# Kernel tuning notes

Measured on AMD Instinct MI355X. Metric: run time of the kernel, lower is better.

## Reference

```python
import jax, jax.numpy as jnp
import numpy as np

B, N, D = 64, 2048, 256
EPS = 1e-05


def setup_inputs() -> dict:
    key = jax.random.key(0)
    k1, k2 = jax.random.split(key)
    x = jax.random.normal(k1, (B, N, D), dtype=jnp.float32)
    lengths = jax.random.randint(k2, (B,), 1, N + 1, dtype=jnp.int32)
    weights = jnp.ones((D,), dtype=jnp.float32)
    biases = jnp.zeros((D,), dtype=jnp.float32)
    return {"x": x, "lengths": lengths, "weights": weights, "biases": biases}


def reference(x, lengths, weights, biases):
    # mask: [B, N, 1], 1.0 for valid set elements (idx < length)
    mask = (jnp.arange(N)[None, :] < lengths[:, None])[..., None].astype(x.dtype)
    denom = (lengths.astype(x.dtype) * D)  # [B]
    xm = x * mask
    means = jnp.sum(xm, axis=(1, 2)) / denom                      # [B]
    x_centered = (xm - means[:, None, None]) * mask               # [B,N,D]
    variances = jnp.sum(x_centered * x_centered, axis=(1, 2)) / denom  # [B]
    x_norm = x_centered / (jnp.sqrt(variances)[:, None, None] + EPS)
    # F.linear(x, diag_embed(w), b) == x * w + b (elementwise per-feature affine)
    out = (x_norm * weights + biases) * mask
    return out
```

## Files before the change

### kernel.cpp

```cpp
#include <hip/hip_runtime.h>


#define BB 64
#define NN 2048
#define DD 256
#define EPSV 1e-5f
#define CHUNKS 32
#define ROWS_PER_CHUNK (NN / CHUNKS)

typedef float f32x4 __attribute__((ext_vector_type(4)));

__global__ __launch_bounds__(256) void setnorm_partials(
    const float* __restrict__ x, const int* __restrict__ lengths,
    float* __restrict__ partials) {
  const int c = blockIdx.x;
  const int b = blockIdx.y;
  const int len = lengths[b];
  const int rowBase = c * ROWS_PER_CHUNK;
  int validRows = len - rowBase;
  if (validRows > ROWS_PER_CHUNK) validRows = ROWS_PER_CHUNK;

  float sum = 0.f, sumsq = 0.f;
  if (validRows > 0) {
    const f32x4* p =
        (const f32x4*)(x + ((size_t)b * NN + (size_t)rowBase) * DD);
    const int n4 = validRows * (DD / 4);
    for (int i = threadIdx.x; i < n4; i += 512) {
      f32x4 v = p[i];
      sum += v.x + v.y + v.z + v.w;
      sumsq += v.x * v.x + v.y * v.y + v.z * v.z + v.w * v.w;
      const int j = i + 256;
      if (j < n4) {
        f32x4 u = p[j];
        sum += u.x + u.y + u.z + u.w;
        sumsq += u.x * u.x + u.y * u.y + u.z * u.z + u.w * u.w;
      }
    }
  }
  #pragma unroll
  for (int off = 32; off > 0; off >>= 1) {
    sum += __shfl_down(sum, off, 64);
    sumsq += __shfl_down(sumsq, off, 64);
  }
  __shared__ float ssum[4], ssq[4];
  const int wave = threadIdx.x >> 6;
  const int lane = threadIdx.x & 63;
  if (lane == 0) { ssum[wave] = sum; ssq[wave] = sumsq; }
  __syncthreads();
  if (threadIdx.x == 0) {
    float ts = 0.f, tq = 0.f;
    #pragma unroll
    for (int w = 0; w < 4; ++w) { ts += ssum[w]; tq += ssq[w]; }
    partials[(b * CHUNKS + c) * 2 + 0] = ts;
    partials[(b * CHUNKS + c) * 2 + 1] = tq;
  }
}

__global__ __launch_bounds__(256) void setnorm_norm(
    const float* __restrict__ x, const int* __restrict__ lengths,
    const float* __restrict__ weights, const float* __restrict__ biases,
    const float* __restrict__ partials, float* __restrict__ out) {
  const int blockBase = blockIdx.x * 1024;
  const int b = blockBase >> 17;
  const int row0 = (blockBase & 131071) >> 6;
  const int len = lengths[b];

  if (row0 >= len) {
    const f32x4 z = {0.f, 0.f, 0.f, 0.f};
    #pragma unroll
    for (int i = 0; i < 4; ++i)
      __builtin_nontemporal_store(z,
          ((f32x4*)out) + blockBase + i * 256 + threadIdx.x);
    return;
  }

  __shared__ float s_mean, s_inv;
  if (threadIdx.x < 64) {
    float s = 0.f, q = 0.f;
    if (threadIdx.x < CHUNKS) {
      s = partials[(b * CHUNKS + threadIdx.x) * 2 + 0];
      q = partials[(b * CHUNKS + threadIdx.x) * 2 + 1];
    }
    #pragma unroll
    for (int off = 16; off > 0; off >>= 1) {
      s += __shfl_down(s, off, 64);
      q += __shfl_down(q, off, 64);
    }
    if (threadIdx.x == 0) {
      const float denom = (float)lengths[b] * (float)DD;
      const float mean = s / denom;
      float var = q / denom - mean * mean;
      var = fmaxf(var, 0.f);
      s_mean = mean;
      s_inv = 1.f / (sqrtf(var) + EPSV);
    }
  }
  __syncthreads();
  const float mean = s_mean;
  const float inv = s_inv;

  const int d4 = threadIdx.x & 63;
  const f32x4 w = ((const f32x4*)weights)[d4];
  const f32x4 bi = ((const f32x4*)biases)[d4];
  const int rowT = row0 + (threadIdx.x >> 6);

  #pragma unroll
  for (int i = 0; i < 4; ++i) {
    const int idx4 = blockBase + i * 256 + threadIdx.x;
    const int row = rowT + i * 4;
    f32x4 o = {0.f, 0.f, 0.f, 0.f};
    if (row < len) {
      const f32x4 v = ((const f32x4*)x)[idx4];
      o.x = (v.x - mean) * inv * w.x + bi.x;
      o.y = (v.y - mean) * inv * w.y + bi.y;
      o.z = (v.z - mean) * inv * w.z + bi.z;
      o.w = (v.w - mean) * inv * w.w + bi.w;
    }
    __builtin_nontemporal_store(o, ((f32x4*)out) + idx4);
  }
}

extern "C" void kernel_launch(void* const* d_in, const int* in_sizes, int n_in,
                              void* d_out, int out_size, void* d_ws, size_t ws_size,
                              hipStream_t stream) {
  const float* x = (const float*)d_in[0];
  const int* lengths = (const int*)d_in[1];
  const float* weights = (const float*)d_in[2];
  const float* biases = (const float*)d_in[3];
  float* out = (float*)d_out;

  float* partials = (float*)d_ws;

  dim3 g1(CHUNKS, BB);
  setnorm_partials<<<g1, 256, 0, stream>>>(x, lengths, partials);
  const int total4 = BB * NN * DD / 4;
  setnorm_norm<<<total4 / 1024, 256, 0, stream>>>(x, lengths, weights, biases,
                                                  partials, out);
}
```

Before: 228.4 us.

## Fuse stats and normalize passes into one cooperative kernel with grid sync

Replaces the two-kernel pipeline with a single cooperative kernel. Each block reduces its chunk's sum and sum of squares, writes partials, waits at a grid-wide barrier, then normalizes the same chunk. The intent is to remove a kernel launch and to reuse the chunk while it may still sit in L2 or the MALL cache, instead of streaming x twice from HBM. The cost is the grid sync overhead and the requirement that all 2048 blocks be resident at once, with the two-kernel path kept as a fallback if the cooperative launch fails.

```diff
diff --git a/kernel.cpp b/kernel.cpp
--- a/kernel.cpp
+++ b/kernel.cpp
@@ -1,4 +1,7 @@
 #include <hip/hip_runtime.h>
+#include <hip/hip_cooperative_groups.h>
+
+namespace cg = cooperative_groups;
 
 
 #define BB 64
@@ -7,8 +10,118 @@
 #define EPSV 1e-5f
 #define CHUNKS 32
 #define ROWS_PER_CHUNK (NN / CHUNKS)
+#define NBLOCKS (BB * CHUNKS)
 
 typedef float f32x4 __attribute__((ext_vector_type(4)));
+
+__global__ __launch_bounds__(256, 8) void setnorm_fused(
+    const float* __restrict__ x, const int* __restrict__ lengths,
+    const float* __restrict__ weights, const float* __restrict__ biases,
+    float* __restrict__ partials, float* __restrict__ out) {
+  const int blk = blockIdx.x;
+  const int b = blk >> 5;
+  const int c = blk & 31;
+  const int len = lengths[b];
+  const int rowBase = c * ROWS_PER_CHUNK;
+  const size_t chunkBase4 = ((size_t)b * NN + (size_t)rowBase) * (DD / 4);
+
+  int validRows = len - rowBase;
+  if (validRows > ROWS_PER_CHUNK) validRows = ROWS_PER_CHUNK;
+
+  if (validRows <= 0) {
+    const f32x4 z = {0.f, 0.f, 0.f, 0.f};
+    f32x4* po = (f32x4*)out + chunkBase4;
+    #pragma unroll 4
+    for (int k = 0; k < 16; ++k)
+      __builtin_nontemporal_store(z, po + k * 256 + threadIdx.x);
+    cg::this_grid().sync();
+    return;
+  }
+
+  float sum = 0.f, sumsq = 0.f;
+  {
+    const f32x4* p = (const f32x4*)x + chunkBase4;
+    const int n4 = validRows * (DD / 4);
+    for (int i = threadIdx.x; i < n4; i += 512) {
+      f32x4 v = p[i];
+      sum += v.x + v.y + v.z + v.w;
+      sumsq += v.x * v.x + v.y * v.y + v.z * v.z + v.w * v.w;
+      const int j = i + 256;
+      if (j < n4) {
+        f32x4 u = p[j];
+        sum += u.x + u.y + u.z + u.w;
+        sumsq += u.x * u.x + u.y * u.y + u.z * u.z + u.w * u.w;
+      }
+    }
+  }
+  #pragma unroll
+  for (int off = 32; off > 0; off >>= 1) {
+    sum += __shfl_down(sum, off, 64);
+    sumsq += __shfl_down(sumsq, off, 64);
+  }
+  __shared__ float ssum[4], ssq[4];
+  {
+    const int wave = threadIdx.x >> 6;
+    const int lane = threadIdx.x & 63;
+    if (lane == 0) { ssum[wave] = sum; ssq[wave] = sumsq; }
+  }
+  __syncthreads();
+  if (threadIdx.x == 0) {
+    const float ts = ssum[0] + ssum[1] + ssum[2] + ssum[3];
+    const float tq = ssq[0] + ssq[1] + ssq[2] + ssq[3];
+    partials[blk * 2 + 0] = ts;
+    partials[blk * 2 + 1] = tq;
+  }
+  __threadfence();
+  cg::this_grid().sync();
+
+  __shared__ float s_mean, s_inv;
+  if (threadIdx.x < 64) {
+    float s = 0.f, q = 0.f;
+    if (threadIdx.x < CHUNKS && threadIdx.x * ROWS_PER_CHUNK < len) {
+      s = partials[(b * CHUNKS + threadIdx.x) * 2 + 0];
+      q = partials[(b * CHUNKS + threadIdx.x) * 2 + 1];
+    }
+    #pragma unroll
+    for (int off = 16; off > 0; off >>= 1) {
+      s += __shfl_down(s, off, 64);
+      q += __shfl_down(q, off, 64);
+    }
+    if (threadIdx.x == 0) {
+      const float denom = (float)len * (float)DD;
+      const float mean = s / denom;
+      float var = q / denom - mean * mean;
+      var = fmaxf(var, 0.f);
+      s_mean = mean;
+      s_inv = 1.f / (sqrtf(var) + EPSV);
+    }
+  }
+  __syncthreads();
+  const float mean = s_mean;
+  const float inv = s_inv;
+
+  const int d4 = threadIdx.x & 63;
+  const f32x4 w = ((const f32x4*)weights)[d4];
+  const f32x4 bi = ((const f32x4*)biases)[d4];
+  const int rowT = rowBase + (threadIdx.x >> 6);
+
+  const f32x4* px = (const f32x4*)x + chunkBase4;
+  f32x4* po = (f32x4*)out + chunkBase4;
+  #pragma unroll 4
+  for (int k = 0; k < 16; ++k) {
+    const int i = k * 256 + threadIdx.x;
+    const int row = rowT + k * 4;
+    f32x4 o = {0.f, 0.f, 0.f, 0.f};
+    if (row < len) {
+      const f32x4 v = px[i];
+      o.x = (v.x - mean) * inv * w.x + bi.x;
+      o.y = (v.y - mean) * inv * w.y + bi.y;
+      o.z = (v.z - mean) * inv * w.z + bi.z;
+      o.w = (v.w - mean) * inv * w.w + bi.w;
+    }
+    __builtin_nontemporal_store(o, po + i);
+  }
+}
 
 __global__ __launch_bounds__(256) void setnorm_partials(
     const float* __restrict__ x, const int* __restrict__ lengths,
@@ -128,12 +241,17 @@
   const float* weights = (const float*)d_in[2];
   const float* biases = (const float*)d_in[3];
   float* out = (float*)d_out;
-
   float* partials = (float*)d_ws;
 
-  dim3 g1(CHUNKS, BB);
-  setnorm_partials<<<g1, 256, 0, stream>>>(x, lengths, partials);
-  const int total4 = BB * NN * DD / 4;
-  setnorm_norm<<<total4 / 1024, 256, 0, stream>>>(x, lengths, weights, biases,
-                                                  partials, out);
-}
+  void* args[] = {(void*)&x, (void*)&lengths, (void*)&weights,
+                  (void*)&biases, (void*)&partials, (void*)&out};
+  const hipError_t err = hipLaunchCooperativeKernel(
+      (const void*)setnorm_fused, dim3(NBLOCKS), dim3(256), args, 0, stream);
+  if (err != hipSuccess) {
+    dim3 g1(CHUNKS, BB);
+    setnorm_partials<<<g1, 256, 0, stream>>>(x, lengths, partials);
+    const int total4 = BB * NN * DD / 4;
+    setnorm_norm<<<total4 / 1024, 256, 0, stream>>>(x, lengths, weights,
+                                                    biases, partials, out);
+  }
+}
```

New measurement: 624.4 us. +173.4%, slower.

## Interleave row groups across blocks and add separate stats finalize kernel

Applied to the files above, without the earlier changes.

The partial-sum kernel now assigns 4-row groups to chunks round-robin instead of contiguous row ranges, so every chunk does a similar amount of valid work whatever the length. A new tiny kernel reduces the per-chunk partials into mean and inverse std once per batch, so the normalize kernel no longer repeats that reduction and barrier in every block. The normalize kernel also strides row groups across blocks so each block gets a mix of valid and padding rows. This balances load across blocks, but costs an extra kernel launch and drops the early-exit path for fully padded blocks.

```diff
diff --git a/kernel.cpp b/kernel.cpp
--- a/kernel.cpp
+++ b/kernel.cpp
@@ -6,7 +6,9 @@
 #define DD 256
 #define EPSV 1e-5f
 #define CHUNKS 32
-#define ROWS_PER_CHUNK (NN / CHUNKS)
+#define GROUPS (NN / 4)
+#define BAT4 (NN * DD / 4)
+#define K2_BPB (GROUPS / 4)
 
 typedef float f32x4 __attribute__((ext_vector_type(4)));
 
@@ -16,25 +18,21 @@
   const int c = blockIdx.x;
   const int b = blockIdx.y;
   const int len = lengths[b];
-  const int rowBase = c * ROWS_PER_CHUNK;
-  int validRows = len - rowBase;
-  if (validRows > ROWS_PER_CHUNK) validRows = ROWS_PER_CHUNK;
+  const int tRow = threadIdx.x >> 6;
+  const int g4 = (len + 3) >> 2;
+  int nk = (g4 - c + 31) >> 5;
+  if (nk < 0) nk = 0;
 
   float sum = 0.f, sumsq = 0.f;
-  if (validRows > 0) {
-    const f32x4* p =
-        (const f32x4*)(x + ((size_t)b * NN + (size_t)rowBase) * DD);
-    const int n4 = validRows * (DD / 4);
-    for (int i = threadIdx.x; i < n4; i += 512) {
-      f32x4 v = p[i];
+  const f32x4* px = (const f32x4*)x + (size_t)b * BAT4;
+  #pragma unroll 4
+  for (int k = 0; k < nk; ++k) {
+    const int g = c + (k << 5);
+    const f32x4 v = px[g * 256 + threadIdx.x];
+    const int row = (g << 2) + tRow;
+    if (row < len) {
       sum += v.x + v.y + v.z + v.w;
       sumsq += v.x * v.x + v.y * v.y + v.z * v.z + v.w * v.w;
-      const int j = i + 256;
-      if (j < n4) {
-        f32x4 u = p[j];
-        sum += u.x + u.y + u.z + u.w;
-        sumsq += u.x * u.x + u.y * u.y + u.z * u.z + u.w * u.w;
-      }
     }
   }
   #pragma unroll
@@ -48,11 +46,33 @@
   if (lane == 0) { ssum[wave] = sum; ssq[wave] = sumsq; }
   __syncthreads();
   if (threadIdx.x == 0) {
-    float ts = 0.f, tq = 0.f;
-    #pragma unroll
-    for (int w = 0; w < 4; ++w) { ts += ssum[w]; tq += ssq[w]; }
+    const float ts = ssum[0] + ssum[1] + ssum[2] + ssum[3];
+    const float tq = ssq[0] + ssq[1] + ssq[2] + ssq[3];
     partials[(b * CHUNKS + c) * 2 + 0] = ts;
     partials[(b * CHUNKS + c) * 2 + 1] = tq;
+  }
+}
+
+__global__ __launch_bounds__(64) void setnorm_finalize(
+    const int* __restrict__ lengths, float* __restrict__ partials) {
+  const int b = blockIdx.x;
+  float s = 0.f, q = 0.f;
+  if (threadIdx.x < CHUNKS) {
+    s = partials[(b * CHUNKS + threadIdx.x) * 2 + 0];
+    q = partials[(b * CHUNKS + threadIdx.x) * 2 + 1];
+  }
+  #pragma unroll
+  for (int off = 16; off > 0; off >>= 1) {
+    s += __shfl_down(s, off, 64);
+    q += __shfl_down(q, off, 64);
+  }
+  if (threadIdx.x == 0) {
+    const float denom = (float)lengths[b] * (float)DD;
+    const float mean = s / denom;
+    float var = q / denom - mean * mean;
+    var = fmaxf(var, 0.f);
+    partials[b * CHUNKS * 2 + 0] = mean;
+    partials[b * CHUNKS * 2 + 1] = 1.f / (sqrtf(var) + EPSV);
   }
 }
 
@@ -60,63 +80,34 @@
     const float* __restrict__ x, const int* __restrict__ lengths,
     const float* __restrict__ weights, const float* __restrict__ biases,
     const float* __restrict__ partials, float* __restrict__ out) {
-  const int blockBase = blockIdx.x * 1024;
-  const int b = blockBase >> 17;
-  const int row0 = (blockBase & 131071) >> 6;
+  const int blk = blockIdx.x;
+  const int b = blk >> 7;
+  const int j = blk & 127;
   const int len = lengths[b];
-
-  if (row0 >= len) {
-    const f32x4 z = {0.f, 0.f, 0.f, 0.f};
-    #pragma unroll
-    for (int i = 0; i < 4; ++i)
-      __builtin_nontemporal_store(z,
-          ((f32x4*)out) + blockBase + i * 256 + threadIdx.x);
-    return;
-  }
-
-  __shared__ float s_mean, s_inv;
-  if (threadIdx.x < 64) {
-    float s = 0.f, q = 0.f;
-    if (threadIdx.x < CHUNKS) {
-      s = partials[(b * CHUNKS + threadIdx.x) * 2 + 0];
-      q = partials[(b * CHUNKS + threadIdx.x) * 2 + 1];
-    }
-    #pragma unroll
-    for (int off = 16; off > 0; off >>= 1) {
-      s += __shfl_down(s, off, 64);
-      q += __shfl_down(q, off, 64);
-    }
-    if (threadIdx.x == 0) {
-      const float denom = (float)lengths[b] * (float)DD;
-      const float mean = s / denom;
-      float var = q / denom - mean * mean;
-      var = fmaxf(var, 0.f);
-      s_mean = mean;
-      s_inv = 1.f / (sqrtf(var) + EPSV);
-    }
-  }
-  __syncthreads();
-  const float mean = s_mean;
-  const float inv = s_inv;
+  const float mean = partials[b * CHUNKS * 2 + 0];
+  const float inv = partials[b * CHUNKS * 2 + 1];
 
   const int d4 = threadIdx.x & 63;
   const f32x4 w = ((const f32x4*)weights)[d4];
   const f32x4 bi = ((const f32x4*)biases)[d4];
-  const int rowT = row0 + (threadIdx.x >> 6);
+  const int tRow = threadIdx.x >> 6;
 
+  const f32x4* px = (const f32x4*)x + (size_t)b * BAT4;
+  f32x4* po = (f32x4*)out + (size_t)b * BAT4;
   #pragma unroll
   for (int i = 0; i < 4; ++i) {
-    const int idx4 = blockBase + i * 256 + threadIdx.x;
-    const int row = rowT + i * 4;
+    const int g = j + (i << 7);
+    const int idx4 = g * 256 + threadIdx.x;
+    const int row = (g << 2) + tRow;
     f32x4 o = {0.f, 0.f, 0.f, 0.f};
     if (row < len) {
-      const f32x4 v = ((const f32x4*)x)[idx4];
+      const f32x4 v = px[idx4];
       o.x = (v.x - mean) * inv * w.x + bi.x;
       o.y = (v.y - mean) * inv * w.y + bi.y;
       o.z = (v.z - mean) * inv * w.z + bi.z;
       o.w = (v.w - mean) * inv * w.w + bi.w;
     }
-    __builtin_nontemporal_store(o, ((f32x4*)out) + idx4);
+    __builtin_nontemporal_store(o, po + idx4);
   }
 }
 
@@ -133,7 +124,7 @@
 
   dim3 g1(CHUNKS, BB);
   setnorm_partials<<<g1, 256, 0, stream>>>(x, lengths, partials);
-  const int total4 = BB * NN * DD / 4;
-  setnorm_norm<<<total4 / 1024, 256, 0, stream>>>(x, lengths, weights, biases,
-                                                  partials, out);
+  setnorm_finalize<<<BB, 64, 0, stream>>>(lengths, partials);
+  setnorm_norm<<<BB * K2_BPB, 256, 0, stream>>>(x, lengths, weights, biases,
+                                                partials, out);
 }
```

Result: no change. 226.5 us (median of 2 runs) (-0.8%).
